# Performance work log

Hardware: AMD Instinct MI355X
Metric: run time of the kernel (lower is better)

Reference implementation:

```python
import math
import jax, jax.numpy as jnp
import numpy as np

B, S, D, H = 4, 2048, 1024, 16
HD = D // H  # head_dim = 64
EPS = 1e-6
LOG2_E = 1.442695041


def setup_inputs() -> dict:
    key = jax.random.key(0)
    ks = jax.random.split(key, 8)
    return {
        "inputs_q": jax.random.normal(ks[0], (B, S, D), dtype=jnp.float32),
        "Wq": jax.random.normal(ks[1], (D, D), dtype=jnp.float32) * 0.02,
        "Wk": jax.random.normal(ks[2], (D, D), dtype=jnp.float32) * 0.02,
        "Wv": jax.random.normal(ks[3], (D, D), dtype=jnp.float32) * 0.02,
        "Wo": jax.random.normal(ks[4], (D, D), dtype=jnp.float32) * 0.02,
        "q_ln_scale": jnp.ones((HD,), dtype=jnp.float32),
        "k_ln_scale": jnp.ones((HD,), dtype=jnp.float32),
        "per_dim_scale": jax.random.normal(ks[5], (HD,), dtype=jnp.float32) * 0.1,
        "patch_mask": jnp.zeros((B, S), dtype=bool),
    }


def _rope(x, position):
    # x: [B, S, H, HD], position: [B, S]
    half = HD // 2
    fraction = 2.0 * jnp.arange(half, dtype=jnp.float32) / HD
    timescale = 1.0 * (10000.0 / 1.0) ** fraction            # [half]
    sinusoid = position[:, :, None, None].astype(jnp.float32) / timescale[None, None, None, :]
    sin, cos = jnp.sin(sinusoid), jnp.cos(sinusoid)
    first, second = jnp.split(x, 2, axis=-1)
    return jnp.concatenate([first * cos - second * sin,
                            second * cos + first * sin], axis=-1)


def _rms_norm(x, scale):
    var = jnp.mean(jnp.square(x), axis=-1, keepdims=True)
    return x * jax.lax.rsqrt(var + EPS) * scale


def reference(inputs_q, Wq, Wk, Wv, Wo, q_ln_scale, k_ln_scale, per_dim_scale, patch_mask):
    b, s, d = inputs_q.shape
    # QKV projections (nn.Linear, no bias): y = x @ W.T
    q = (inputs_q @ Wq.T).reshape(b, s, H, HD)
    k = (inputs_q @ Wk.T).reshape(b, s, H, HD)
    v = (inputs_q @ Wv.T).reshape(b, s, H, HD)

    num_masked = jnp.sum(patch_mask.astype(jnp.int32), axis=-1)  # [B]
    # decode_cache=None => next_index = 0
    position = jnp.arange(s, dtype=jnp.int32)[None, :] - num_masked[:, None]  # [B, S]

    q = _rope(q, position)
    k = _rope(k, position)

    q = _rms_norm(q, q_ln_scale)
    k = _rms_norm(k, k_ln_scale)

    # per-dim scale
    q = q * (LOG2_E / math.sqrt(HD) * jax.nn.softplus(per_dim_scale))

    # causal + prefix-padding mask: [B, 1, S, S]
    q_idx = jnp.arange(s)[None, None, :, None]
    kv_idx = jnp.arange(s)[None, None, None, :]
    mask = (q_idx >= kv_idx) & (kv_idx >= num_masked[:, None, None, None])

    scores = jnp.einsum("bqhd,bkhd->bhqk", q, k)
    neg = -jnp.finfo(scores.dtype).max / 2
    scores = jnp.where(mask, scores, neg)
    attn = jax.nn.softmax(scores, axis=-1)
    x = jnp.einsum("bhqk,bkhd->bqhd", attn, v).reshape(b, s, d)
    return x @ Wo.T
```

## Files before the change

kernel.cpp:

```cpp
#include <hip/hip_runtime.h>
#include <cstdint>
#include <cstddef>

#define BB 4
#define SS 2048
#define DD 1024
#define HH 16

typedef __bf16 bf16;
typedef __bf16 bf16x8 __attribute__((ext_vector_type(8)));
typedef __bf16 bf16x4 __attribute__((ext_vector_type(4)));
typedef float f32x4 __attribute__((ext_vector_type(4)));
typedef unsigned int u32;

typedef __attribute__((address_space(1))) const void* as1_cvoid;
typedef __attribute__((address_space(3))) void* as3_void;

__device__ __forceinline__ void gload_lds16(const void* g, void* l) {
  __builtin_amdgcn_global_load_lds((as1_cvoid)g, (as3_void)l, 16, 0, 0);
}

__global__ void mask_count_kernel(const unsigned char* __restrict__ mask, int* __restrict__ nm) {
  int wid = threadIdx.x >> 6, lane = threadIdx.x & 63;
  if (wid >= BB) return;
  int s = 0;
  for (int i = lane; i < SS; i += 64) s += (mask[wid * SS + i] != 0) ? 1 : 0;
#pragma unroll
  for (int m = 1; m < 64; m <<= 1) s += __shfl_xor(s, m);
  if (lane == 0) nm[wid] = s;
}

__global__ void cvt_kernel(const float* __restrict__ src, bf16* __restrict__ dst, int n4) {
  int stride = gridDim.x * blockDim.x;
  for (int i = blockIdx.x * blockDim.x + threadIdx.x; i < n4; i += stride) {
    float4 v = ((const float4*)src)[i];
    bf16x4 o;
    o[0] = (bf16)v.x; o[1] = (bf16)v.y; o[2] = (bf16)v.z; o[3] = (bf16)v.w;
    ((bf16x4*)dst)[i] = o;
  }
}

__global__ void cvt4_kernel(const float* __restrict__ W0, const float* __restrict__ W1,
                            const float* __restrict__ W2, const float* __restrict__ W3,
                            bf16* __restrict__ D0, bf16* __restrict__ D1,
                            bf16* __restrict__ D2, bf16* __restrict__ D3) {
  int which = blockIdx.x >> 8;
  const float* src = which == 0 ? W0 : which == 1 ? W1 : which == 2 ? W2 : W3;
  bf16* dst = which == 0 ? D0 : which == 1 ? D1 : which == 2 ? D2 : D3;
  const int n4 = DD * DD / 4;
  for (int i = (blockIdx.x & 255) * 256 + threadIdx.x; i < n4; i += 65536) {
    float4 v = ((const float4*)src)[i];
    bf16x4 o;
    o[0] = (bf16)v.x; o[1] = (bf16)v.y; o[2] = (bf16)v.z; o[3] = (bf16)v.w;
    ((bf16x4*)dst)[i] = o;
  }
}

__global__ void sincos_table_kernel(const int* __restrict__ nm, float2* __restrict__ tbl) {
  int g = blockIdx.x * 256 + threadIdx.x;
  int j = g & 31;
  int idx = g >> 5;
  int b = idx >> 11, s = idx & 2047;
  int pos = s - nm[b];
  float inv_ts = __expf((float)j * (-9.210340371976184f / 32.0f));
  float sn, cs;
  sincosf((float)pos * inv_ts, &sn, &cs);
  tbl[g] = make_float2(cs, sn);
}

__global__ void __launch_bounds__(256) gemm_qkv_kernel(
    const bf16* __restrict__ A, const bf16* __restrict__ Wq, const bf16* __restrict__ Wk,
    const bf16* __restrict__ Wv, const float* __restrict__ qls, const float* __restrict__ kls,
    const float* __restrict__ pds, const float2* __restrict__ tbl,
    bf16* __restrict__ Qp, bf16* __restrict__ Kp, bf16* __restrict__ Vt) {
  __shared__ __align__(16) char smem[4 * 64 * 72 * 2];
  bf16* Ab = (bf16*)smem;
  bf16* Bb = (bf16*)(smem + 8192);
  const int tid = threadIdx.x;
  const int wid = tid >> 6, lane = tid & 63;
  const int lr = lane & 15, lg = lane >> 4;
  const int K = DD;
  const int nx = 24;
  const int cpx = gridDim.x >> 3;
  const int lid = (blockIdx.x & 7) * cpx + (blockIdx.x >> 3);
  const int m0 = (lid / nx) * 128;
  const int ntile = lid % nx;
  const int which = ntile >> 3;
  const int n0 = (ntile & 7) * 128;
  const bf16* Bm = which == 0 ? Wq : (which == 1 ? Wk : Wv);
  const int wm = (wid >> 1) * 64, wn = (wid & 1) * 64;
  f32x4 acc[4][4] = {};
  for (int k0 = 0; k0 < K; k0 += 32) {
    __syncthreads();
#pragma unroll
    for (int i = 0; i < 2; ++i) {
      int o = (wid * 2 + i) * 1024 + lane * 16;
      int row = o >> 6;
      int ke = (o & 63) >> 1;
      gload_lds16(A + (size_t)(m0 + row) * K + k0 + ke, (char*)Ab + o);
      gload_lds16(Bm + (size_t)(n0 + row) * K + k0 + ke, (char*)Bb + o);
    }
    __syncthreads();
    bf16x8 af[4], bf_[4];
#pragma unroll
    for (int i = 0; i < 4; ++i) af[i] = *(const bf16x8*)&Ab[(wm + i * 16 + lr) * 32 + lg * 8];
#pragma unroll
    for (int j = 0; j < 4; ++j) bf_[j] = *(const bf16x8*)&Bb[(wn + j * 16 + lr) * 32 + lg * 8];
#pragma unroll
    for (int i = 0; i < 4; ++i)
#pragma unroll
      for (int j = 0; j < 4; ++j)
        acc[i][j] = __builtin_amdgcn_mfma_f32_16x16x32_bf16(af[i], bf_[j], acc[i][j], 0, 0, 0);
  }
  const int b = m0 >> 11;
  const int s0g = m0 & 2047;
  const int hq = n0 >> 6;
  if (which < 2) {
    float scj[4];
#pragma unroll
    for (int j = 0; j < 4; ++j) {
      int d = j * 16 + lr;
      scj[j] = (which == 0) ? qls[d] * 0.26017112262570096f * log1pf(__expf(pds[d]))
                            : kls[d];
    }
    bf16* Out = which == 0 ? Qp : Kp;
    const int h = hq + (wn >> 6);
    const size_t base = (size_t)(b * 16 + h) * SS;
#pragma unroll
    for (int i = 0; i < 4; ++i)
#pragma unroll
      for (int r = 0; r < 4; ++r) {
        int srow = s0g + wm + i * 16 + lg * 4 + r;
        const float2* trow = tbl + ((size_t)(b * SS + srow) << 5);
        float2 t0 = trow[lr], t1 = trow[16 + lr];
        float a0 = acc[i][0][r], a1 = acc[i][1][r], a2 = acc[i][2][r], a3 = acc[i][3][r];
        float n0_ = a0 * t0.x - a2 * t0.y;
        float n2_ = a2 * t0.x + a0 * t0.y;
        float n1_ = a1 * t1.x - a3 * t1.y;
        float n3_ = a3 * t1.x + a1 * t1.y;
        float ssum = n0_ * n0_ + n1_ * n1_ + n2_ * n2_ + n3_ * n3_;
        ssum += __shfl_xor(ssum, 1);
        ssum += __shfl_xor(ssum, 2);
        ssum += __shfl_xor(ssum, 4);
        ssum += __shfl_xor(ssum, 8);
        float rinv = rsqrtf(ssum * (1.0f / 64.0f) + 1e-6f);
        bf16* orow = Out + (base + srow) * 64;
        orow[lr]      = (bf16)(n0_ * rinv * scj[0]);
        orow[16 + lr] = (bf16)(n1_ * rinv * scj[1]);
        orow[32 + lr] = (bf16)(n2_ * rinv * scj[2]);
        orow[48 + lr] = (bf16)(n3_ * rinv * scj[3]);
      }
  } else {
    __syncthreads();
    bf16* tw = (bf16*)smem + wid * 64 * 72;
#pragma unroll
    for (int i = 0; i < 4; ++i)
#pragma unroll
      for (int j = 0; j < 4; ++j)
#pragma unroll
        for (int r = 0; r < 4; ++r)
          tw[(j * 16 + lr) * 72 + i * 16 + lg * 4 + r] = (bf16)acc[i][j][r];
    __syncthreads();
    int d = tid >> 2, sc = (tid & 3) * 16;
#pragma unroll
    for (int w = 0; w < 4; ++w) {
      int rh = w >> 1, hh = w & 1;
      const bf16* ts = (const bf16*)smem + w * 64 * 72 + d * 72 + sc;
      bf16x8 v0 = *(const bf16x8*)ts;
      bf16x8 v1 = *(const bf16x8*)(ts + 8);
      size_t vo = ((size_t)((b * 16 + hq + hh) * 64 + d)) * SS + s0g + rh * 64 + sc;
      *(bf16x8*)(Vt + vo) = v0;
      *(bf16x8*)(Vt + vo + 8) = v1;
    }
  }
}

__global__ void __launch_bounds__(256) gemm_bt_kernel(const bf16* __restrict__ A,
                                                      const bf16* __restrict__ Bm,
                                                      float* __restrict__ Cout,
                                                      int M, int N, int K) {
  __shared__ bf16 Ab[128 * 32];
  __shared__ bf16 Bb[128 * 32];
  const int tid = threadIdx.x;
  const int wid = tid >> 6, lane = tid & 63;
  const int lr = lane & 15, lg = lane >> 4;
  const int nx = N >> 7;
  const int cpx = gridDim.x >> 3;
  const int lid = (blockIdx.x & 7) * cpx + (blockIdx.x >> 3);
  const int m0 = (lid / nx) * 128, n0 = (lid % nx) * 128;
  const int wm = (wid >> 1) * 64, wn = (wid & 1) * 64;
  f32x4 acc[4][4] = {};
  for (int k0 = 0; k0 < K; k0 += 32) {
    __syncthreads();
#pragma unroll
    for (int i = 0; i < 2; ++i) {
      int o = (wid * 2 + i) * 1024 + lane * 16;
      int row = o >> 6;
      int ke = (o & 63) >> 1;
      gload_lds16(A + (size_t)(m0 + row) * K + k0 + ke, (char*)Ab + o);
      gload_lds16(Bm + (size_t)(n0 + row) * K + k0 + ke, (char*)Bb + o);
    }
    __syncthreads();
    bf16x8 af[4], bf_[4];
#pragma unroll
    for (int i = 0; i < 4; ++i) af[i] = *(const bf16x8*)&Ab[(wm + i * 16 + lr) * 32 + lg * 8];
#pragma unroll
    for (int j = 0; j < 4; ++j) bf_[j] = *(const bf16x8*)&Bb[(wn + j * 16 + lr) * 32 + lg * 8];
#pragma unroll
    for (int i = 0; i < 4; ++i)
#pragma unroll
      for (int j = 0; j < 4; ++j)
        acc[i][j] = __builtin_amdgcn_mfma_f32_16x16x32_bf16(af[i], bf_[j], acc[i][j], 0, 0, 0);
  }
#pragma unroll
  for (int i = 0; i < 4; ++i)
#pragma unroll
    for (int j = 0; j < 4; ++j)
#pragma unroll
      for (int r = 0; r < 4; ++r) {
        int row = m0 + wm + i * 16 + lg * 4 + r;
        int col = n0 + wn + j * 16 + lr;
        Cout[(size_t)row * N + col] = acc[i][j][r];
      }
}

__global__ void __launch_bounds__(256, 2) flash_kernel(
    const bf16* __restrict__ Qp, const bf16* __restrict__ Kp, const bf16* __restrict__ Vt,
    bf16* __restrict__ O, const int* __restrict__ nm) {
  __shared__ bf16 Kb[2][64 * 64];
  __shared__ bf16 Vb[64 * 64];
  __shared__ u32 Pl[4][16][32];
  const int bh = blockIdx.x & 63;
  const int px = blockIdx.x >> 6;
  const int xA = 31 - px, xB = px;
  const int b = bh >> 4, h = bh & 15;
  const int tid = threadIdx.x;
  const int wid = tid >> 6, lane = tid & 63;
  const int lr = lane & 15, lg = lane >> 4;
  const int sw = (lr & 7) << 2;
  const int nmb = nm[b];
  const int wqA = xA * 64 + wid * 16;
  const int wqB = xB * 64 + wid * 16;
  const int nt = xA + 1;

  const int koffA = lr * 128 + ((lg ^ (lr & 7)) << 4);
  const int koffB = lr * 128 + (((4 + lg) ^ (lr & 7)) << 4);
  const int o0 = tid * 16, o1 = 4096 + tid * 16;
  const int r0 = o0 >> 7, r1 = o1 >> 7;
  const int c0 = ((o0 >> 4) & 7) ^ (r0 & 7), c1 = ((o1 >> 4) & 7) ^ (r1 & 7);
  const bf16* kg0 = Kp + (size_t)bh * (SS * 64) + r0 * 64 + c0 * 8;
  const bf16* kg1 = Kp + (size_t)bh * (SS * 64) + r1 * 64 + c1 * 8;
  const bf16* vg0 = Vt + (size_t)bh * (SS * 64) + (size_t)r0 * SS + c0 * 8;
  const bf16* vg1 = Vt + (size_t)bh * (SS * 64) + (size_t)r1 * SS + c1 * 8;
  char* kl0 = (char*)&Kb[0][0] + o0;
  char* kl1 = (char*)&Kb[0][0] + o1;
  char* vl0 = (char*)Vb + o0;
  char* vl1 = (char*)Vb + o1;
  u32* plw = &Pl[wid][lr][0];

  bf16x8 qfA[2], qfB[2];
#pragma unroll
  for (int kh = 0; kh < 2; ++kh) {
    qfA[kh] = *(const bf16x8*)(Qp + ((size_t)bh * SS + wqA + lr) * 64 + kh * 32 + lg * 8);
    qfB[kh] = *(const bf16x8*)(Qp + ((size_t)bh * SS + wqB + lr) * 64 + kh * 32 + lg * 8);
  }

  float mA = -1e30f, lA = 0.f, mB = -1e30f, lB = 0.f;
  f32x4 oA[4] = {}, oB[4] = {};

  auto STAGE_K = [&](int bi, int t) {
    gload_lds16(kg0 + (size_t)t * 4096, kl0 + bi * 8192);
    gload_lds16(kg1 + (size_t)t * 4096, kl1 + bi * 8192);
  };
  auto STAGE_V = [&](int t) {
    gload_lds16(vg0 + t * 64, vl0);
    gload_lds16(vg1 + t * 64, vl1);
  };

  STAGE_K(0, 0);
  STAGE_V(0);
  __syncthreads();
  int buf = 0;
  for (int t = 0; t < nt; ++t) {
    const int kv0 = t * 64;
    if (t + 1 < nt) STAGE_K(buf ^ 1, t + 1);
    const bool actB = (t <= xB);
    f32x4 sA[4], sB[4];

    const char* kbb = (const char*)&Kb[0][0] + buf * 8192;
    __builtin_amdgcn_s_setprio(1);
#pragma unroll
    for (int j = 0; j < 4; ++j) {
      bf16x8 kf0 = *(const bf16x8*)(kbb + koffA + j * 2048);
      bf16x8 kf1 = *(const bf16x8*)(kbb + koffB + j * 2048);
      f32x4 z = {};
      z = __builtin_amdgcn_mfma_f32_16x16x32_bf16(kf0, qfA[0], z, 0, 0, 0);
      z = __builtin_amdgcn_mfma_f32_16x16x32_bf16(kf1, qfA[1], z, 0, 0, 0);
      sA[j] = z;
      if (actB) {
        f32x4 z2 = {};
        z2 = __builtin_amdgcn_mfma_f32_16x16x32_bf16(kf0, qfB[0], z2, 0, 0, 0);
        z2 = __builtin_amdgcn_mfma_f32_16x16x32_bf16(kf1, qfB[1], z2, 0, 0, 0);
        sB[j] = z2;
      }
    }
    __builtin_amdgcn_s_setprio(0);

    auto SOFTMAX = [&](f32x4* s, float& m_r, float& l_pp, f32x4* oacc, bf16x8* pb,
                       int xS, int wqS) {
      if (t == xS) {
        int qr = wqS + lr;
#pragma unroll
        for (int j = 0; j < 4; ++j) {
          int kvb = kv0 + j * 16 + lg * 4;
#pragma unroll
          for (int r = 0; r < 4; ++r)
            if (kvb + r > qr) s[j][r] = -1e30f;
        }
      }
      if (kv0 < nmb) {
#pragma unroll
        for (int j = 0; j < 4; ++j) {
          int kvb = kv0 + j * 16 + lg * 4;
#pragma unroll
          for (int r = 0; r < 4; ++r)
            if (kvb + r < nmb) s[j][r] = -1e30f;
        }
      }
      float t0 = fmaxf(fmaxf(s[0][0], s[0][1]), s[0][2]);
      float t1 = fmaxf(fmaxf(s[0][3], s[1][0]), s[1][1]);
      float t2 = fmaxf(fmaxf(s[1][2], s[1][3]), s[2][0]);
      float t3 = fmaxf(fmaxf(s[2][1], s[2][2]), s[2][3]);
      float t4 = fmaxf(fmaxf(s[3][0], s[3][1]), s[3][2]);
      float t5 = fmaxf(fmaxf(t0, t1), s[3][3]);
      float pm = fmaxf(fmaxf(t2, t3), fmaxf(t4, t5));
      if (!__all(pm - m_r <= 8.f)) {
        pm = fmaxf(pm, __shfl_xor(pm, 16));
        pm = fmaxf(pm, __shfl_xor(pm, 32));
        float mn = fmaxf(m_r, pm);
        float scl = exp2f(m_r - mn);
        m_r = mn;
        l_pp *= scl;
        f32x4 sv = {scl, scl, scl, scl};
#pragma unroll
        for (int jd = 0; jd < 4; ++jd) oacc[jd] *= sv;
      }
      const float mloc = m_r;
      float lp = l_pp;
#pragma unroll
      for (int j = 0; j < 4; ++j) {
        float p0 = exp2f(s[j][0] - mloc), p1 = exp2f(s[j][1] - mloc);
        float p2 = exp2f(s[j][2] - mloc), p3 = exp2f(s[j][3] - mloc);
        lp += (p0 + p1) + (p2 + p3);
        union { bf16 hx[4]; uint2 u2; } pk;
        pk.hx[0] = (bf16)p0; pk.hx[1] = (bf16)p1;
        pk.hx[2] = (bf16)p2; pk.hx[3] = (bf16)p3;
        *(uint2*)&plw[(j * 8 + lg * 2) ^ sw] = pk.u2;
      }
      l_pp = lp;
#pragma unroll
      for (int kh = 0; kh < 2; ++kh)
        pb[kh] = *(const bf16x8*)&plw[(kh * 16 + lg * 4) ^ sw];
    };

    bf16x8 pbA[2], pbB[2];
    SOFTMAX(sA, mA, lA, oA, pbA, xA, wqA);
    if (actB) SOFTMAX(sB, mB, lB, oB, pbB, xB, wqB);

    if (t > 0) {
      if (t + 1 < nt)
        asm volatile("s_waitcnt vmcnt(2)" ::: "memory");
      else
        asm volatile("s_waitcnt vmcnt(0)" ::: "memory");
      __builtin_amdgcn_s_barrier();
      __builtin_amdgcn_sched_barrier(0);
    }
    __builtin_amdgcn_s_setprio(1);
#pragma unroll
    for (int jd = 0; jd < 4; ++jd) {
      bf16x8 va0 = *(const bf16x8*)((const char*)Vb + koffA + jd * 2048);
      bf16x8 va1 = *(const bf16x8*)((const char*)Vb + koffB + jd * 2048);
      oA[jd] = __builtin_amdgcn_mfma_f32_16x16x32_bf16(va0, pbA[0], oA[jd], 0, 0, 0);
      oA[jd] = __builtin_amdgcn_mfma_f32_16x16x32_bf16(va1, pbA[1], oA[jd], 0, 0, 0);
      if (actB) {
        oB[jd] = __builtin_amdgcn_mfma_f32_16x16x32_bf16(va0, pbB[0], oB[jd], 0, 0, 0);
        oB[jd] = __builtin_amdgcn_mfma_f32_16x16x32_bf16(va1, pbB[1], oB[jd], 0, 0, 0);
      }
    }
    __builtin_amdgcn_s_setprio(0);
    __syncthreads();
    if (t + 1 < nt) STAGE_V(t + 1);
    buf ^= 1;
  }
#pragma unroll
  for (int st = 0; st < 2; ++st) {
    float l = st == 0 ? lA : lB;
    const f32x4* oacc = st == 0 ? oA : oB;
    int wq = st == 0 ? wqA : wqB;
    l += __shfl_xor(l, 16);
    l += __shfl_xor(l, 32);
    float invl = 1.0f / l;
    size_t rowoff = ((size_t)b * SS + wq + lr) * DD + h * 64;
#pragma unroll
    for (int jd = 0; jd < 4; ++jd) {
      f32x4 ov = oacc[jd] * invl;
      bf16x4 hv;
      hv[0] = (bf16)ov[0]; hv[1] = (bf16)ov[1]; hv[2] = (bf16)ov[2]; hv[3] = (bf16)ov[3];
      *(bf16x4*)(O + rowoff + jd * 16 + lg * 4) = hv;
    }
  }
}

extern "C" void kernel_launch(void* const* d_in, const int* in_sizes, int n_in,
                              void* d_out, int out_size, void* d_ws, size_t ws_size,
                              hipStream_t stream) {
  const float* X = (const float*)d_in[0];
  const float* Wq = (const float*)d_in[1];
  const float* Wk = (const float*)d_in[2];
  const float* Wv = (const float*)d_in[3];
  const float* Wo = (const float*)d_in[4];
  const float* qls = (const float*)d_in[5];
  const float* kls = (const float*)d_in[6];
  const float* pds = (const float*)d_in[7];
  const unsigned char* mask = (const unsigned char*)d_in[8];

  char* ws = (char*)d_ws;
  size_t off = 0;
  auto alloc = [&](size_t bytes) {
    char* p = ws + off;
    off += (bytes + 255) & ~(size_t)255;
    return p;
  };
  const size_t NTOK = (size_t)BB * SS;
  int* nm = (int*)alloc(16);
  bf16* Xb = (bf16*)alloc(NTOK * DD * 2);
  bf16* Wqb = (bf16*)alloc((size_t)DD * DD * 2);
  bf16* Wkb = (bf16*)alloc((size_t)DD * DD * 2);
  bf16* Wvb = (bf16*)alloc((size_t)DD * DD * 2);
  bf16* Wob = (bf16*)alloc((size_t)DD * DD * 2);
  bf16* Qp = (bf16*)alloc(NTOK * DD * 2);
  bf16* Kp = (bf16*)alloc(NTOK * DD * 2);
  bf16* Vt = (bf16*)alloc(NTOK * DD * 2);
  float2* tbl = (float2*)alloc(NTOK * 32 * sizeof(float2));
  bf16* Oat = Xb;

  mask_count_kernel<<<1, 256, 0, stream>>>(mask, nm);
  cvt_kernel<<<1024, 256, 0, stream>>>(X, Xb, (int)(NTOK * DD / 4));
  cvt4_kernel<<<1024, 256, 0, stream>>>(Wq, Wk, Wv, Wo, Wqb, Wkb, Wvb, Wob);
  sincos_table_kernel<<<1024, 256, 0, stream>>>(nm, tbl);

  gemm_qkv_kernel<<<(int)(NTOK / 128) * 24, 256, 0, stream>>>(Xb, Wqb, Wkb, Wvb, qls, kls, pds,
                                                              tbl, Qp, Kp, Vt);
  flash_kernel<<<1024, 256, 0, stream>>>(Qp, Kp, Vt, Oat, nm);
  gemm_bt_kernel<<<(int)(NTOK / 128) * (DD / 128), 256, 0, stream>>>(Oat, Wob, (float*)d_out,
                                                                     (int)NTOK, DD, DD);
}
```

Before: 197.2 us.

## Restructure QKV GEMM into 256x128 tiles with double-buffered async LDS pipeline

The QKV projection GEMM now uses 512-thread blocks on 256x128 output tiles with BK=64. Global-to-LDS loads are double-buffered and prefetched two k-steps ahead, gated by explicit vmcnt waits and raw barriers instead of full __syncthreads around every load. LDS columns are XOR-swizzled to avoid bank conflicts, and MFMA sections are raised to higher priority. The V-transpose epilogue is simplified to per-wave writes without block syncs. The cost is 96KB of LDS per block, which limits occupancy, plus hand-tuned wait counts that must match the issue order.

Result: slower. 206.7 us (+4.8%).

```diff
diff --git a/kernel.cpp b/kernel.cpp
--- a/kernel.cpp
+++ b/kernel.cpp
@@ -68,53 +68,87 @@
   tbl[g] = make_float2(cs, sn);
 }
 
-__global__ void __launch_bounds__(256) gemm_qkv_kernel(
+__global__ void __launch_bounds__(512) gemm_qkv_kernel(
     const bf16* __restrict__ A, const bf16* __restrict__ Wq, const bf16* __restrict__ Wk,
     const bf16* __restrict__ Wv, const float* __restrict__ qls, const float* __restrict__ kls,
     const float* __restrict__ pds, const float2* __restrict__ tbl,
     bf16* __restrict__ Qp, bf16* __restrict__ Kp, bf16* __restrict__ Vt) {
-  __shared__ __align__(16) char smem[4 * 64 * 72 * 2];
-  bf16* Ab = (bf16*)smem;
-  bf16* Bb = (bf16*)(smem + 8192);
+  __shared__ __align__(16) char smem[98304];
   const int tid = threadIdx.x;
   const int wid = tid >> 6, lane = tid & 63;
   const int lr = lane & 15, lg = lane >> 4;
-  const int K = DD;
+  const int wr = wid >> 1, wc = wid & 1;
   const int nx = 24;
   const int cpx = gridDim.x >> 3;
   const int lid = (blockIdx.x & 7) * cpx + (blockIdx.x >> 3);
-  const int m0 = (lid / nx) * 128;
+  const int m0 = (lid / nx) * 256;
   const int ntile = lid % nx;
   const int which = ntile >> 3;
   const int n0 = (ntile & 7) * 128;
   const bf16* Bm = which == 0 ? Wq : (which == 1 ? Wk : Wv);
-  const int wm = (wid >> 1) * 64, wn = (wid & 1) * 64;
+
+  const int srow = tid >> 2;
+  const int gsw = (tid & 3) ^ (srow & 3);
+  const bf16* Ag0 = A + (size_t)(m0 + srow) * DD + gsw * 8;
+  const bf16* Ag1 = A + (size_t)(m0 + 128 + srow) * DD + gsw * 8;
+  const bf16* Bg = Bm + (size_t)(n0 + srow) * DD + gsw * 8;
+  char* Al = smem + tid * 16;
+  char* Bl = smem + 65536 + tid * 16;
+
+  auto STAGE = [&](int bufb, int kh, int t) {
+    const int ko = t * 64 + kh * 32;
+    char* ab = Al + bufb * 32768 + kh * 16384;
+    gload_lds16(Ag0 + ko, ab);
+    gload_lds16(Ag1 + ko, ab + 8192);
+    gload_lds16(Bg + ko, Bl + bufb * 16384 + kh * 8192);
+  };
+
+  const int aoff = (wr * 64 + lr) * 64 + ((lg ^ (lr & 3)) << 4);
+  const int boff = 65536 + (wc * 64 + lr) * 64 + ((lg ^ (lr & 3)) << 4);
+
   f32x4 acc[4][4] = {};
-  for (int k0 = 0; k0 < K; k0 += 32) {
-    __syncthreads();
-#pragma unroll
-    for (int i = 0; i < 2; ++i) {
-      int o = (wid * 2 + i) * 1024 + lane * 16;
-      int row = o >> 6;
-      int ke = (o & 63) >> 1;
-      gload_lds16(A + (size_t)(m0 + row) * K + k0 + ke, (char*)Ab + o);
-      gload_lds16(Bm + (size_t)(n0 + row) * K + k0 + ke, (char*)Bb + o);
-    }
-    __syncthreads();
-    bf16x8 af[4], bf_[4];
-#pragma unroll
-    for (int i = 0; i < 4; ++i) af[i] = *(const bf16x8*)&Ab[(wm + i * 16 + lr) * 32 + lg * 8];
-#pragma unroll
-    for (int j = 0; j < 4; ++j) bf_[j] = *(const bf16x8*)&Bb[(wn + j * 16 + lr) * 32 + lg * 8];
-#pragma unroll
-    for (int i = 0; i < 4; ++i)
-#pragma unroll
-      for (int j = 0; j < 4; ++j)
-        acc[i][j] = __builtin_amdgcn_mfma_f32_16x16x32_bf16(af[i], bf_[j], acc[i][j], 0, 0, 0);
-  }
+  const int nt = DD / 64;
+  STAGE(0, 0, 0);
+  STAGE(0, 1, 0);
+  STAGE(1, 0, 1);
+  STAGE(1, 1, 1);
+  for (int t = 0; t < nt; ++t) {
+    const int buf = t & 1;
+#pragma unroll
+    for (int kh = 0; kh < 2; ++kh) {
+      if (kh == 0) {
+        if (t < nt - 1) asm volatile("s_waitcnt vmcnt(9)" ::: "memory");
+        else            asm volatile("s_waitcnt vmcnt(3)" ::: "memory");
+      } else {
+        if (t < nt - 2)       asm volatile("s_waitcnt vmcnt(9)" ::: "memory");
+        else if (t == nt - 2) asm volatile("s_waitcnt vmcnt(6)" ::: "memory");
+        else                  asm volatile("s_waitcnt vmcnt(0)" ::: "memory");
+      }
+      __builtin_amdgcn_s_barrier();
+      __builtin_amdgcn_sched_barrier(0);
+      const char* ap = smem + buf * 32768 + kh * 16384 + aoff;
+      const char* bp = smem + buf * 16384 + kh * 8192 + boff;
+      bf16x8 af[4], bf_[4];
+#pragma unroll
+      for (int f = 0; f < 4; ++f) af[f] = *(const bf16x8*)(ap + f * 1024);
+#pragma unroll
+      for (int c = 0; c < 4; ++c) bf_[c] = *(const bf16x8*)(bp + c * 1024);
+      __builtin_amdgcn_s_setprio(1);
+#pragma unroll
+      for (int f = 0; f < 4; ++f)
+#pragma unroll
+        for (int c = 0; c < 4; ++c)
+          acc[f][c] = __builtin_amdgcn_mfma_f32_16x16x32_bf16(af[f], bf_[c], acc[f][c], 0, 0, 0);
+      __builtin_amdgcn_s_setprio(0);
+      __builtin_amdgcn_sched_barrier(0);
+      __builtin_amdgcn_s_barrier();
+      if (t < nt - 2) STAGE(buf, kh, t + 2);
+    }
+  }
+
   const int b = m0 >> 11;
   const int s0g = m0 & 2047;
-  const int hq = n0 >> 6;
+  const int h = (n0 >> 6) + wc;
   if (which < 2) {
     float scj[4];
 #pragma unroll
@@ -124,14 +158,13 @@
                             : kls[d];
     }
     bf16* Out = which == 0 ? Qp : Kp;
-    const int h = hq + (wn >> 6);
     const size_t base = (size_t)(b * 16 + h) * SS;
 #pragma unroll
     for (int i = 0; i < 4; ++i)
 #pragma unroll
       for (int r = 0; r < 4; ++r) {
-        int srow = s0g + wm + i * 16 + lg * 4 + r;
-        const float2* trow = tbl + ((size_t)(b * SS + srow) << 5);
+        int srw = s0g + wr * 64 + i * 16 + lg * 4 + r;
+        const float2* trow = tbl + ((size_t)(b * SS + srw) << 5);
         float2 t0 = trow[lr], t1 = trow[16 + lr];
         float a0 = acc[i][0][r], a1 = acc[i][1][r], a2 = acc[i][2][r], a3 = acc[i][3][r];
         float n0_ = a0 * t0.x - a2 * t0.y;
@@ -144,14 +177,13 @@
         ssum += __shfl_xor(ssum, 4);
         ssum += __shfl_xor(ssum, 8);
         float rinv = rsqrtf(ssum * (1.0f / 64.0f) + 1e-6f);
-        bf16* orow = Out + (base + srow) * 64;
+        bf16* orow = Out + (base + srw) * 64;
         orow[lr]      = (bf16)(n0_ * rinv * scj[0]);
         orow[16 + lr] = (bf16)(n1_ * rinv * scj[1]);
         orow[32 + lr] = (bf16)(n2_ * rinv * scj[2]);
         orow[48 + lr] = (bf16)(n3_ * rinv * scj[3]);
       }
   } else {
-    __syncthreads();
     bf16* tw = (bf16*)smem + wid * 64 * 72;
 #pragma unroll
     for (int i = 0; i < 4; ++i)
@@ -160,18 +192,12 @@
 #pragma unroll
         for (int r = 0; r < 4; ++r)
           tw[(j * 16 + lr) * 72 + i * 16 + lg * 4 + r] = (bf16)acc[i][j][r];
-    __syncthreads();
-    int d = tid >> 2, sc = (tid & 3) * 16;
-#pragma unroll
-    for (int w = 0; w < 4; ++w) {
-      int rh = w >> 1, hh = w & 1;
-      const bf16* ts = (const bf16*)smem + w * 64 * 72 + d * 72 + sc;
-      bf16x8 v0 = *(const bf16x8*)ts;
-      bf16x8 v1 = *(const bf16x8*)(ts + 8);
-      size_t vo = ((size_t)((b * 16 + hq + hh) * 64 + d)) * SS + s0g + rh * 64 + sc;
-      *(bf16x8*)(Vt + vo) = v0;
-      *(bf16x8*)(Vt + vo + 8) = v1;
-    }
+    const int d = lane;
+    const bf16* ts = tw + d * 72;
+    size_t vo = ((size_t)((b * 16 + h) * 64 + d)) * SS + s0g + wr * 64;
+#pragma unroll
+    for (int w = 0; w < 8; ++w)
+      *(bf16x8*)(Vt + vo + w * 8) = *(const bf16x8*)(ts + w * 8);
   }
 }
 
@@ -449,8 +475,7 @@
   cvt4_kernel<<<1024, 256, 0, stream>>>(Wq, Wk, Wv, Wo, Wqb, Wkb, Wvb, Wob);
   sincos_table_kernel<<<1024, 256, 0, stream>>>(nm, tbl);
 
-  gemm_qkv_kernel<<<(int)(NTOK / 128) * 24, 256, 0, stream>>>(Xb, Wqb, Wkb, Wvb, qls, kls, pds,
-                                                              tbl, Qp, Kp, Vt);
+  gemm_qkv_kernel<<<768, 512, 0, stream>>>(Xb, Wqb, Wkb, Wvb, qls, kls, pds, tbl, Qp, Kp, Vt);
   flash_kernel<<<1024, 256, 0, stream>>>(Qp, Kp, Vt, Oat, nm);
   gemm_bt_kernel<<<(int)(NTOK / 128) * (DD / 128), 256, 0, stream>>>(Oat, Wob, (float*)d_out,
                                                                      (int)NTOK, DD, DD);
```
